# Kernel tuning notes

Hardware: AMD Instinct MI355X
Metric: run time of the kernel (lower is better)

Reference implementation:

```python
import jax, jax.numpy as jnp
import numpy as np

N, M, E = 100000, 50000, 1600000
C_IN, C_OUT = 128, 128
BN_EPS = 1e-5


def setup_inputs() -> dict:
    key = jax.random.key(0)
    ks = jax.random.split(key, 10)
    ref_bxyz = jax.random.normal(ks[0], (N, 4), dtype=jnp.float32)
    ref_feat = jax.random.normal(ks[1], (N, C_IN), dtype=jnp.float32)
    query_bxyz = jax.random.normal(ks[2], (M, 4), dtype=jnp.float32)
    e_ref = jax.random.randint(ks[3], (E,), 0, N)
    e_query = jax.random.randint(ks[4], (E,), 0, M)
    # pos_encoder: Linear(3, C_OUT); mlp: Linear(C_IN, C_OUT); BatchNorm1d(C_OUT)
    W_pos = jax.random.normal(ks[5], (C_OUT, 3), dtype=jnp.float32) / np.sqrt(3.0)
    b_pos = jnp.zeros((C_OUT,), dtype=jnp.float32)
    W_mlp = jax.random.normal(ks[6], (C_OUT, C_IN), dtype=jnp.float32) / np.sqrt(C_IN)
    b_mlp = jnp.zeros((C_OUT,), dtype=jnp.float32)
    gamma = jnp.ones((C_OUT,), dtype=jnp.float32)
    beta = jnp.zeros((C_OUT,), dtype=jnp.float32)
    return {
        "ref_bxyz": ref_bxyz, "ref_feat": ref_feat, "query_bxyz": query_bxyz,
        "e_ref": e_ref, "e_query": e_query,
        "W_pos": W_pos, "b_pos": b_pos, "W_mlp": W_mlp, "b_mlp": b_mlp,
        "gamma": gamma, "beta": beta,
    }


def reference(ref_bxyz, ref_feat, query_bxyz, e_ref, e_query,
              W_pos, b_pos, W_mlp, b_mlp, gamma, beta):
    num_q = query_bxyz.shape[0]
    # gather endpoints, xyz difference (drop batch-index column 0)
    pos_diff = (ref_bxyz[e_ref] - query_bxyz[e_query])[:, 1:4]          # [E, 3]
    pos_embedding = pos_diff @ W_pos.T + b_pos                           # [E, C_OUT]
    output_feat = (ref_feat @ W_mlp.T + b_mlp)[e_ref]                   # [E, C_OUT]
    # scatter-mean into queries (empty segments -> 0, clamp count at 1)
    s = jax.ops.segment_sum(pos_embedding + output_feat, e_query, num_segments=num_q)
    cnt = jax.ops.segment_sum(jnp.ones((e_query.shape[0],), pos_embedding.dtype),
                              e_query, num_segments=num_q)
    query_feat = s / jnp.maximum(cnt, 1.0)[:, None]                     # [M, C_OUT]
    # BatchNorm1d (training-mode batch stats, biased variance) + ReLU
    mu = jnp.mean(query_feat, axis=0)
    var = jnp.mean(jnp.square(query_feat - mu), axis=0)
    normed = (query_feat - mu) * jax.lax.rsqrt(var + BN_EPS) * gamma + beta
    return jax.nn.relu(normed)
```

## Files before the change

### kernel.cpp

```cpp
#include <hip/hip_runtime.h>


__device__ __forceinline__ float bf_lo(unsigned u) {
  union { unsigned u; float f; } c; c.u = u << 16; return c.f;
}
__device__ __forceinline__ float bf_hi(unsigned u) {
  union { unsigned u; float f; } c; c.u = u & 0xFFFF0000u; return c.f;
}
__device__ __forceinline__ unsigned pack_bf(float x, float y) {
  union { float f; unsigned u; } a, b; a.f = x; b.f = y;
  unsigned lo = (a.u + 0x7FFFu + ((a.u >> 16) & 1u)) >> 16;
  unsigned hi = (b.u + 0x7FFFu + ((b.u >> 16) & 1u)) >> 16;
  return lo | (hi << 16);
}

__global__ __launch_bounds__(256) void k_cvt(const float4* __restrict__ in,
                                             uint4* __restrict__ outb, int n8) {
  int i = blockIdx.x * blockDim.x + threadIdx.x;
  if (i < n8) {
    float4 a = in[2 * i], b = in[2 * i + 1];
    uint4 o;
    o.x = pack_bf(a.x, a.y);
    o.y = pack_bf(a.z, a.w);
    o.z = pack_bf(b.x, b.y);
    o.w = pack_bf(b.z, b.w);
    outb[i] = o;
  }
}

__global__ void k_build(const int* __restrict__ eq, const int* __restrict__ er,
                        int* __restrict__ head, int2* __restrict__ node, int E_) {
  int i = blockIdx.x * blockDim.x + threadIdx.x;
  if (i < E_) {
    int q = eq[i];
    int prev = atomicExch(&head[q], i);
    node[i] = make_int2(prev, er[i]);
  }
}

__global__ __launch_bounds__(256) void k_accum_b(const int* __restrict__ head,
                                                 const int2* __restrict__ node,
                                                 const uint4* __restrict__ featb,
                                                 const float* __restrict__ bxyz,
                                                 float4* __restrict__ accF4,
                                                 float* __restrict__ possum, int M_) {
  int q = blockIdx.x * 16 + (threadIdx.x >> 4);
  int l = threadIdx.x & 15;
  if (q >= M_) return;
  int i = head[q];
  float a0 = 0.f, a1 = 0.f, a2 = 0.f, a3 = 0.f;
  float a4 = 0.f, a5 = 0.f, a6 = 0.f, a7 = 0.f;
  float p = 0.f, c = 0.f;
  while (i >= 0) {
    int2 nd = node[i];
    int r = nd.y;
    uint4 v = featb[(size_t)r * 16 + l];
    a0 += bf_lo(v.x); a1 += bf_hi(v.x);
    a2 += bf_lo(v.y); a3 += bf_hi(v.y);
    a4 += bf_lo(v.z); a5 += bf_hi(v.z);
    a6 += bf_lo(v.w); a7 += bf_hi(v.w);
    if (l < 3) p += bxyz[r * 4 + 1 + l];
    c += 1.f;
    i = nd.x;
  }
  float4 o0 = make_float4(a0, a1, a2, a3);
  float4 o1 = make_float4(a4, a5, a6, a7);
  accF4[(size_t)q * 32 + l * 2] = o0;
  accF4[(size_t)q * 32 + l * 2 + 1] = o1;
  if (l < 3) possum[q * 4 + l] = p;
  if (l == 3) possum[q * 4 + 3] = c;
}

__global__ __launch_bounds__(256) void k_accum(const int* __restrict__ head,
                                               const int2* __restrict__ node,
                                               const float4* __restrict__ feat4,
                                               const float* __restrict__ bxyz,
                                               float4* __restrict__ accF4,
                                               float* __restrict__ possum, int M_) {
  int q = blockIdx.x * 8 + (threadIdx.x >> 5);
  int l = threadIdx.x & 31;
  if (q >= M_) return;
  int i = head[q];
  float4 a = make_float4(0.f, 0.f, 0.f, 0.f);
  float p = 0.f, c = 0.f;
  while (i >= 0) {
    int2 nd = node[i];
    int r = nd.y;
    float4 v = feat4[(size_t)r * 32 + l];
    a.x += v.x; a.y += v.y; a.z += v.z; a.w += v.w;
    if (l < 3) p += bxyz[r * 4 + 1 + l];
    c += 1.f;
    i = nd.x;
  }
  accF4[(size_t)q * 32 + l] = a;
  if (l < 3) possum[q * 4 + l] = p;
  if (l == 3) possum[q * 4 + 3] = c;
}

__global__ __launch_bounds__(256) void k_gemm(
    const float* __restrict__ accF, const float4* __restrict__ possum4,
    const float* __restrict__ qxyz,
    const float* __restrict__ Wm, const float* __restrict__ Wp,
    const float* __restrict__ bm, const float* __restrict__ bp,
    float* __restrict__ out, int M_) {
  __shared__ float sA[32 * 132];
  __shared__ float sW[128 * 36];
  int t = threadIdx.x;
  int q0 = blockIdx.x * 32;
  #pragma unroll
  for (int i = 0; i < 4; ++i) {
    int f = t + 256 * i;
    int q = f >> 5;
    int kk = (f & 31) << 2;
    float4 v = make_float4(0.f, 0.f, 0.f, 0.f);
    if (q0 + q < M_) v = *(const float4*)&accF[(q0 + q) * 128 + kk];
    *(float4*)&sA[q * 132 + kk] = v;
  }
  float acc[4][4];
  #pragma unroll
  for (int i = 0; i < 4; ++i)
    #pragma unroll
    for (int j = 0; j < 4; ++j) acc[i][j] = 0.f;
  int q0l = (t >> 5) << 2;
  int cb = t & 31;
  for (int kt = 0; kt < 4; ++kt) {
    __syncthreads();
    #pragma unroll
    for (int i = 0; i < 4; ++i) {
      int f = t + 256 * i;
      int c = f >> 3;
      int kk = (f & 7) << 2;
      float4 v = *(const float4*)&Wm[c * 128 + kt * 32 + kk];
      *(float4*)&sW[c * 36 + kk] = v;
    }
    __syncthreads();
    #pragma unroll
    for (int kk4 = 0; kk4 < 8; ++kk4) {
      float4 av[4], wv[4];
      #pragma unroll
      for (int i = 0; i < 4; ++i)
        av[i] = *(const float4*)&sA[(q0l + i) * 132 + kt * 32 + (kk4 << 2)];
      #pragma unroll
      for (int j = 0; j < 4; ++j)
        wv[j] = *(const float4*)&sW[(cb + 32 * j) * 36 + (kk4 << 2)];
      #pragma unroll
      for (int i = 0; i < 4; ++i)
        #pragma unroll
        for (int j = 0; j < 4; ++j) {
          acc[i][j] = fmaf(av[i].x, wv[j].x, acc[i][j]);
          acc[i][j] = fmaf(av[i].y, wv[j].y, acc[i][j]);
          acc[i][j] = fmaf(av[i].z, wv[j].z, acc[i][j]);
          acc[i][j] = fmaf(av[i].w, wv[j].w, acc[i][j]);
        }
    }
  }
  float fcnt[4], inv[4], dx[4], dy[4], dz[4];
  #pragma unroll
  for (int i = 0; i < 4; ++i) {
    int q = q0 + q0l + i;
    if (q < M_) {
      float4 ps = possum4[q];
      float fc = ps.w;
      fcnt[i] = fc;
      inv[i] = 1.f / fmaxf(fc, 1.f);
      dx[i] = ps.x - fc * qxyz[q * 4 + 1];
      dy[i] = ps.y - fc * qxyz[q * 4 + 2];
      dz[i] = ps.z - fc * qxyz[q * 4 + 3];
    } else {
      fcnt[i] = 0.f; inv[i] = 1.f; dx[i] = dy[i] = dz[i] = 0.f;
    }
  }
  #pragma unroll
  for (int j = 0; j < 4; ++j) {
    int c = cb + 32 * j;
    float w0 = Wp[c * 3 + 0], w1 = Wp[c * 3 + 1], w2 = Wp[c * 3 + 2];
    float bb = bm[c] + bp[c];
    #pragma unroll
    for (int i = 0; i < 4; ++i) {
      int q = q0 + q0l + i;
      if (q < M_) {
        float v = acc[i][j] + dx[i] * w0 + dy[i] * w1 + dz[i] * w2 + fcnt[i] * bb;
        out[q * 128 + c] = v * inv[i];
      }
    }
  }
}

__global__ __launch_bounds__(256) void k_stats(const float* __restrict__ qf,
                                               float* __restrict__ stats, int M_) {
  __shared__ float ls[256], ls2[256];
  int c = threadIdx.x & 127;
  int half = threadIdx.x >> 7;
  int rpb = (M_ + gridDim.x - 1) / gridDim.x;
  int r0 = blockIdx.x * rpb;
  int r1 = r0 + rpb; if (r1 > M_) r1 = M_;
  float s = 0.f, s2 = 0.f;
  for (int r = r0 + half; r < r1; r += 2) {
    float v = qf[r * 128 + c];
    s += v; s2 += v * v;
  }
  ls[threadIdx.x] = s; ls2[threadIdx.x] = s2;
  __syncthreads();
  if (half == 0) {
    s += ls[threadIdx.x + 128];
    s2 += ls2[threadIdx.x + 128];
    atomicAdd(&stats[c], s);
    atomicAdd(&stats[128 + c], s2);
  }
}

__global__ void k_bnprep(float* __restrict__ stats, const float* __restrict__ gamma,
                         const float* __restrict__ beta, int M_) {
  int c = threadIdx.x;
  float inv_m = 1.f / (float)M_;
  float mu = stats[c] * inv_m;
  float var = stats[128 + c] * inv_m - mu * mu;
  var = fmaxf(var, 0.f);
  float sc = gamma[c] * rsqrtf(var + 1e-5f);
  stats[256 + c] = sc;
  stats[384 + c] = beta[c] - mu * sc;
}

__global__ __launch_bounds__(256) void k_bnapply(float* __restrict__ out,
                                                 const float* __restrict__ stats, int total4) {
  const float4* sc4 = (const float4*)(stats + 256);
  const float4* sh4 = (const float4*)(stats + 384);
  float4* o4 = (float4*)out;
  for (int i = blockIdx.x * blockDim.x + threadIdx.x; i < total4;
       i += gridDim.x * blockDim.x) {
    float4 v = o4[i];
    float4 s = sc4[i & 31];
    float4 h = sh4[i & 31];
    v.x = fmaxf(fmaf(v.x, s.x, h.x), 0.f);
    v.y = fmaxf(fmaf(v.y, s.y, h.y), 0.f);
    v.z = fmaxf(fmaf(v.z, s.z, h.z), 0.f);
    v.w = fmaxf(fmaf(v.w, s.w, h.w), 0.f);
    o4[i] = v;
  }
}

static inline size_t align256(size_t x) { return (x + 255) & ~(size_t)255; }

extern "C" void kernel_launch(void* const* d_in, const int* in_sizes, int n_in,
                              void* d_out, int out_size, void* d_ws, size_t ws_size,
                              hipStream_t stream) {
  const float* ref_bxyz   = (const float*)d_in[0];
  const float* ref_feat   = (const float*)d_in[1];
  const float* query_bxyz = (const float*)d_in[2];
  const int*   e_ref      = (const int*)d_in[3];
  const int*   e_query    = (const int*)d_in[4];
  const float* W_pos      = (const float*)d_in[5];
  const float* b_pos      = (const float*)d_in[6];
  const float* W_mlp      = (const float*)d_in[7];
  const float* b_mlp      = (const float*)d_in[8];
  const float* gamma      = (const float*)d_in[9];
  const float* beta       = (const float*)d_in[10];

  int N_ = in_sizes[0] / 4;
  int M_ = in_sizes[2] / 4;
  int E_ = in_sizes[3];

  char* ws = (char*)d_ws;
  size_t off = 0;
  int*   head   = (int*)(ws + off);   off += align256((size_t)M_ * 4);
  int2*  node   = (int2*)(ws + off);  off += align256((size_t)E_ * 8);
  float* possum = (float*)(ws + off); off += align256((size_t)M_ * 4 * 4);
  float* accF   = (float*)(ws + off); off += align256((size_t)M_ * 128 * 4);
  float* stats  = (float*)(ws + off); off += align256(4 * 128 * 4);
  uint4* featb  = (uint4*)(ws + off);
  size_t need_b = off + align256((size_t)N_ * 128 * 2);
  bool use_bf16 = (need_b <= ws_size);

  hipMemsetAsync(head, 0xFF, (size_t)M_ * 4, stream);
  hipMemsetAsync(stats, 0, 2 * 128 * 4, stream);

  float* out = (float*)d_out;

  if (use_bf16) {
    int n8 = N_ * 16;
    k_cvt<<<(n8 + 255) / 256, 256, 0, stream>>>((const float4*)ref_feat, featb, n8);
  }
  k_build<<<(E_ + 255) / 256, 256, 0, stream>>>(e_query, e_ref, head, node, E_);
  if (use_bf16) {
    k_accum_b<<<(M_ + 15) / 16, 256, 0, stream>>>(head, node, featb, ref_bxyz,
                                                  (float4*)accF, possum, M_);
  } else {
    k_accum<<<(M_ + 7) / 8, 256, 0, stream>>>(head, node, (const float4*)ref_feat,
                                              ref_bxyz, (float4*)accF, possum, M_);
  }
  k_gemm<<<(M_ + 31) / 32, 256, 0, stream>>>(accF, (const float4*)possum, query_bxyz,
                                             W_mlp, W_pos, b_mlp, b_pos, out, M_);
  k_stats<<<256, 256, 0, stream>>>(out, stats, M_);
  k_bnprep<<<1, 128, 0, stream>>>(stats, gamma, beta, M_);
  k_bnapply<<<2048, 256, 0, stream>>>(out, stats, M_ * 32);
}
```

Baseline: 383.3 us.

## Fuse conversion with list build, BN stats into GEMM, BN prep into apply

Merges the bf16 conversion and the linked-list build into a single launch. Computes per-channel BatchNorm sums inside the GEMM epilogue via a shared-memory reduction and atomics, and folds the scale/shift prep into the apply kernel. It also drops the fp32 fallback path and changes the shared W tile to a float2 layout with stride 34. This removes two kernel launches and a full re-read of the output for statistics, at the cost of more atomics per GEMM block and an unconditional assumption that the bf16 workspace fits.

```diff
diff --git a/kernel.cpp b/kernel.cpp
--- a/kernel.cpp
+++ b/kernel.cpp
@@ -14,23 +14,21 @@
   return lo | (hi << 16);
 }
 
-__global__ __launch_bounds__(256) void k_cvt(const float4* __restrict__ in,
-                                             uint4* __restrict__ outb, int n8) {
+__global__ __launch_bounds__(256) void k_build_cvt(
+    const int* __restrict__ eq, const int* __restrict__ er,
+    int* __restrict__ head, int2* __restrict__ node,
+    const float4* __restrict__ featf, uint4* __restrict__ featb,
+    int E_, int n8) {
   int i = blockIdx.x * blockDim.x + threadIdx.x;
   if (i < n8) {
-    float4 a = in[2 * i], b = in[2 * i + 1];
+    float4 a = featf[2 * i], b = featf[2 * i + 1];
     uint4 o;
     o.x = pack_bf(a.x, a.y);
     o.y = pack_bf(a.z, a.w);
     o.z = pack_bf(b.x, b.y);
     o.w = pack_bf(b.z, b.w);
-    outb[i] = o;
-  }
-}
-
-__global__ void k_build(const int* __restrict__ eq, const int* __restrict__ er,
-                        int* __restrict__ head, int2* __restrict__ node, int E_) {
-  int i = blockIdx.x * blockDim.x + threadIdx.x;
+    featb[i] = o;
+  }
   if (i < E_) {
     int q = eq[i];
     int prev = atomicExch(&head[q], i);
@@ -71,40 +69,14 @@
   if (l == 3) possum[q * 4 + 3] = c;
 }
 
-__global__ __launch_bounds__(256) void k_accum(const int* __restrict__ head,
-                                               const int2* __restrict__ node,
-                                               const float4* __restrict__ feat4,
-                                               const float* __restrict__ bxyz,
-                                               float4* __restrict__ accF4,
-                                               float* __restrict__ possum, int M_) {
-  int q = blockIdx.x * 8 + (threadIdx.x >> 5);
-  int l = threadIdx.x & 31;
-  if (q >= M_) return;
-  int i = head[q];
-  float4 a = make_float4(0.f, 0.f, 0.f, 0.f);
-  float p = 0.f, c = 0.f;
-  while (i >= 0) {
-    int2 nd = node[i];
-    int r = nd.y;
-    float4 v = feat4[(size_t)r * 32 + l];
-    a.x += v.x; a.y += v.y; a.z += v.z; a.w += v.w;
-    if (l < 3) p += bxyz[r * 4 + 1 + l];
-    c += 1.f;
-    i = nd.x;
-  }
-  accF4[(size_t)q * 32 + l] = a;
-  if (l < 3) possum[q * 4 + l] = p;
-  if (l == 3) possum[q * 4 + 3] = c;
-}
-
 __global__ __launch_bounds__(256) void k_gemm(
     const float* __restrict__ accF, const float4* __restrict__ possum4,
     const float* __restrict__ qxyz,
     const float* __restrict__ Wm, const float* __restrict__ Wp,
     const float* __restrict__ bm, const float* __restrict__ bp,
-    float* __restrict__ out, int M_) {
+    float* __restrict__ out, float* __restrict__ stats, int M_) {
   __shared__ float sA[32 * 132];
-  __shared__ float sW[128 * 36];
+  __shared__ float sW[128 * 34];
   int t = threadIdx.x;
   int q0 = blockIdx.x * 32;
   #pragma unroll
@@ -123,34 +95,39 @@
     for (int j = 0; j < 4; ++j) acc[i][j] = 0.f;
   int q0l = (t >> 5) << 2;
   int cb = t & 31;
+  float2* sW2 = (float2*)sW;
+  const float2* Wm2 = (const float2*)Wm;
   for (int kt = 0; kt < 4; ++kt) {
     __syncthreads();
     #pragma unroll
-    for (int i = 0; i < 4; ++i) {
+    for (int i = 0; i < 8; ++i) {
       int f = t + 256 * i;
-      int c = f >> 3;
-      int kk = (f & 7) << 2;
-      float4 v = *(const float4*)&Wm[c * 128 + kt * 32 + kk];
-      *(float4*)&sW[c * 36 + kk] = v;
+      int c = f >> 4;
+      int kk2 = f & 15;
+      sW2[c * 17 + kk2] = Wm2[c * 64 + kt * 16 + kk2];
     }
     __syncthreads();
     #pragma unroll
     for (int kk4 = 0; kk4 < 8; ++kk4) {
-      float4 av[4], wv[4];
+      float4 av[4];
+      float2 wa[4], wb[4];
       #pragma unroll
       for (int i = 0; i < 4; ++i)
         av[i] = *(const float4*)&sA[(q0l + i) * 132 + kt * 32 + (kk4 << 2)];
       #pragma unroll
-      for (int j = 0; j < 4; ++j)
-        wv[j] = *(const float4*)&sW[(cb + 32 * j) * 36 + (kk4 << 2)];
+      for (int j = 0; j < 4; ++j) {
+        int c = cb + 32 * j;
+        wa[j] = sW2[c * 17 + kk4 * 2];
+        wb[j] = sW2[c * 17 + kk4 * 2 + 1];
+      }
       #pragma unroll
       for (int i = 0; i < 4; ++i)
         #pragma unroll
         for (int j = 0; j < 4; ++j) {
-          acc[i][j] = fmaf(av[i].x, wv[j].x, acc[i][j]);
-          acc[i][j] = fmaf(av[i].y, wv[j].y, acc[i][j]);
-          acc[i][j] = fmaf(av[i].z, wv[j].z, acc[i][j]);
-          acc[i][j] = fmaf(av[i].w, wv[j].w, acc[i][j]);
+          acc[i][j] = fmaf(av[i].x, wa[j].x, acc[i][j]);
+          acc[i][j] = fmaf(av[i].y, wa[j].y, acc[i][j]);
+          acc[i][j] = fmaf(av[i].z, wb[j].x, acc[i][j]);
+          acc[i][j] = fmaf(av[i].w, wb[j].y, acc[i][j]);
         }
     }
   }
@@ -170,63 +147,66 @@
       fcnt[i] = 0.f; inv[i] = 1.f; dx[i] = dy[i] = dz[i] = 0.f;
     }
   }
+  float psum[4], psq[4];
   #pragma unroll
   for (int j = 0; j < 4; ++j) {
     int c = cb + 32 * j;
     float w0 = Wp[c * 3 + 0], w1 = Wp[c * 3 + 1], w2 = Wp[c * 3 + 2];
     float bb = bm[c] + bp[c];
+    float s = 0.f, s2 = 0.f;
     #pragma unroll
     for (int i = 0; i < 4; ++i) {
       int q = q0 + q0l + i;
-      if (q < M_) {
-        float v = acc[i][j] + dx[i] * w0 + dy[i] * w1 + dz[i] * w2 + fcnt[i] * bb;
-        out[q * 128 + c] = v * inv[i];
-      }
-    }
-  }
-}
-
-__global__ __launch_bounds__(256) void k_stats(const float* __restrict__ qf,
-                                               float* __restrict__ stats, int M_) {
-  __shared__ float ls[256], ls2[256];
-  int c = threadIdx.x & 127;
-  int half = threadIdx.x >> 7;
-  int rpb = (M_ + gridDim.x - 1) / gridDim.x;
-  int r0 = blockIdx.x * rpb;
-  int r1 = r0 + rpb; if (r1 > M_) r1 = M_;
-  float s = 0.f, s2 = 0.f;
-  for (int r = r0 + half; r < r1; r += 2) {
-    float v = qf[r * 128 + c];
-    s += v; s2 += v * v;
-  }
-  ls[threadIdx.x] = s; ls2[threadIdx.x] = s2;
+      float v = acc[i][j] + dx[i] * w0 + dy[i] * w1 + dz[i] * w2 + fcnt[i] * bb;
+      float val = v * inv[i];
+      if (q >= M_) val = 0.f;
+      if (q < M_) out[q * 128 + c] = val;
+      s += val; s2 += val * val;
+    }
+    psum[j] = s; psq[j] = s2;
+  }
   __syncthreads();
-  if (half == 0) {
-    s += ls[threadIdx.x + 128];
-    s2 += ls2[threadIdx.x + 128];
-    atomicAdd(&stats[c], s);
-    atomicAdd(&stats[128 + c], s2);
-  }
-}
-
-__global__ void k_bnprep(float* __restrict__ stats, const float* __restrict__ gamma,
-                         const float* __restrict__ beta, int M_) {
-  int c = threadIdx.x;
-  float inv_m = 1.f / (float)M_;
-  float mu = stats[c] * inv_m;
-  float var = stats[128 + c] * inv_m - mu * mu;
-  var = fmaxf(var, 0.f);
-  float sc = gamma[c] * rsqrtf(var + 1e-5f);
-  stats[256 + c] = sc;
-  stats[384 + c] = beta[c] - mu * sc;
+  float* red = sA;
+  int rg = t >> 5;
+  #pragma unroll
+  for (int j = 0; j < 4; ++j) {
+    int c = cb + 32 * j;
+    red[c * 8 + rg] = psum[j];
+    red[1024 + c * 8 + rg] = psq[j];
+  }
+  __syncthreads();
+  if (t < 128) {
+    float s = 0.f, s2 = 0.f;
+    #pragma unroll
+    for (int r = 0; r < 8; ++r) {
+      s += red[t * 8 + r];
+      s2 += red[1024 + t * 8 + r];
+    }
+    atomicAdd(&stats[t], s);
+    atomicAdd(&stats[128 + t], s2);
+  }
 }
 
 __global__ __launch_bounds__(256) void k_bnapply(float* __restrict__ out,
-                                                 const float* __restrict__ stats, int total4) {
-  const float4* sc4 = (const float4*)(stats + 256);
-  const float4* sh4 = (const float4*)(stats + 384);
+                                                 const float* __restrict__ stats,
+                                                 const float* __restrict__ gamma,
+                                                 const float* __restrict__ beta,
+                                                 float inv_m, int total4) {
+  __shared__ float sc[128], sh[128];
+  int t = threadIdx.x;
+  if (t < 128) {
+    float mu = stats[t] * inv_m;
+    float var = stats[128 + t] * inv_m - mu * mu;
+    var = fmaxf(var, 0.f);
+    float s = gamma[t] * rsqrtf(var + 1e-5f);
+    sc[t] = s;
+    sh[t] = beta[t] - mu * s;
+  }
+  __syncthreads();
+  const float4* sc4 = (const float4*)sc;
+  const float4* sh4 = (const float4*)sh;
   float4* o4 = (float4*)out;
-  for (int i = blockIdx.x * blockDim.x + threadIdx.x; i < total4;
+  for (int i = blockIdx.x * blockDim.x + t; i < total4;
        i += gridDim.x * blockDim.x) {
     float4 v = o4[i];
     float4 s = sc4[i & 31];
@@ -266,31 +246,22 @@
   int2*  node   = (int2*)(ws + off);  off += align256((size_t)E_ * 8);
   float* possum = (float*)(ws + off); off += align256((size_t)M_ * 4 * 4);
   float* accF   = (float*)(ws + off); off += align256((size_t)M_ * 128 * 4);
-  float* stats  = (float*)(ws + off); off += align256(4 * 128 * 4);
+  float* stats  = (float*)(ws + off); off += align256(2 * 128 * 4);
   uint4* featb  = (uint4*)(ws + off);
-  size_t need_b = off + align256((size_t)N_ * 128 * 2);
-  bool use_bf16 = (need_b <= ws_size);
 
   hipMemsetAsync(head, 0xFF, (size_t)M_ * 4, stream);
   hipMemsetAsync(stats, 0, 2 * 128 * 4, stream);
 
   float* out = (float*)d_out;
-
-  if (use_bf16) {
-    int n8 = N_ * 16;
-    k_cvt<<<(n8 + 255) / 256, 256, 0, stream>>>((const float4*)ref_feat, featb, n8);
-  }
-  k_build<<<(E_ + 255) / 256, 256, 0, stream>>>(e_query, e_ref, head, node, E_);
-  if (use_bf16) {
-    k_accum_b<<<(M_ + 15) / 16, 256, 0, stream>>>(head, node, featb, ref_bxyz,
-                                                  (float4*)accF, possum, M_);
-  } else {
-    k_accum<<<(M_ + 7) / 8, 256, 0, stream>>>(head, node, (const float4*)ref_feat,
-                                              ref_bxyz, (float4*)accF, possum, M_);
-  }
+  int n8 = N_ * 16;
+  int nwork = (E_ > n8) ? E_ : n8;
+
+  k_build_cvt<<<(nwork + 255) / 256, 256, 0, stream>>>(
+      e_query, e_ref, head, node, (const float4*)ref_feat, featb, E_, n8);
+  k_accum_b<<<(M_ + 15) / 16, 256, 0, stream>>>(head, node, featb, ref_bxyz,
+                                                (float4*)accF, possum, M_);
   k_gemm<<<(M_ + 31) / 32, 256, 0, stream>>>(accF, (const float4*)possum, query_bxyz,
-                                             W_mlp, W_pos, b_mlp, b_pos, out, M_);
-  k_stats<<<256, 256, 0, stream>>>(out, stats, M_);
-  k_bnprep<<<1, 128, 0, stream>>>(stats, gamma, beta, M_);
-  k_bnapply<<<2048, 256, 0, stream>>>(out, stats, M_ * 32);
-}
+                                             W_mlp, W_pos, b_mlp, b_pos, out, stats, M_);
+  k_bnapply<<<2048, 256, 0, stream>>>(out, stats, gamma, beta, 1.f / (float)M_,
+                                      M_ * 32);
+}
```

New measurement: 353.1 us. -7.9%, faster.
